# Kernel tuning notes

Measured on AMD Instinct MI355X. Metric: run time of the kernel, lower is better.

The kernel has to match this reference:

```python
import jax, jax.numpy as jnp
import numpy as np

B, S, D, H, F = 8, 1024, 1024, 16, 4096
DH = D // H  # 64
EPS = 1e-5


def layer_norm(x, g, b):
    mu = jnp.mean(x, axis=-1, keepdims=True)
    var = jnp.mean(jnp.square(x - mu), axis=-1, keepdims=True)
    return (x - mu) * jax.lax.rsqrt(var + EPS) * g + b


def mha(q_in, k_in, v_in, wq, wk, wv, wo, causal):
    # wq/wk/wv: [H, D, DH] (stacked per-head nn.Linear weights, pre-transposed)
    Q = jnp.einsum('bsd,hdk->bhsk', q_in, wq)
    K = jnp.einsum('bsd,hdk->bhsk', k_in, wk)
    V = jnp.einsum('bsd,hdk->bhsk', v_in, wv)
    scores = jnp.einsum('bhsk,bhtk->bhst', Q, K) / jnp.sqrt(jnp.asarray(DH, Q.dtype))
    if causal:
        mask = jnp.triu(jnp.ones((S, S), dtype=bool), k=1)  # True = inaccessible
        scores = jnp.where(mask, -jnp.inf, scores)
    A = jax.nn.softmax(scores, axis=-1)
    heads = jnp.einsum('bhst,bhtk->bhsk', A, V)
    heads = heads.transpose(0, 2, 1, 3).reshape(q_in.shape[0], q_in.shape[1], D)
    return heads @ wo.T  # nn.Linear convention


def setup_inputs() -> dict:
    key = jax.random.key(0)
    ks = jax.random.split(key, 16)
    sc = 1.0 / np.sqrt(D)
    scf = 1.0 / np.sqrt(F)
    return {
        'embeds': jax.random.normal(ks[0], (B, S, D), jnp.float32),
        'encoder_output': jax.random.normal(ks[1], (B, S, D), jnp.float32),
        'wq1': jax.random.normal(ks[2], (H, D, DH), jnp.float32) * sc,
        'wk1': jax.random.normal(ks[3], (H, D, DH), jnp.float32) * sc,
        'wv1': jax.random.normal(ks[4], (H, D, DH), jnp.float32) * sc,
        'wo1': jax.random.normal(ks[5], (D, D), jnp.float32) * sc,
        'wq2': jax.random.normal(ks[6], (H, D, DH), jnp.float32) * sc,
        'wk2': jax.random.normal(ks[7], (H, D, DH), jnp.float32) * sc,
        'wv2': jax.random.normal(ks[8], (H, D, DH), jnp.float32) * sc,
        'wo2': jax.random.normal(ks[9], (D, D), jnp.float32) * sc,
        'ln1_g': jnp.ones((D,), jnp.float32), 'ln1_b': jnp.zeros((D,), jnp.float32),
        'ln2_g': jnp.ones((D,), jnp.float32), 'ln2_b': jnp.zeros((D,), jnp.float32),
        'ln3_g': jnp.ones((D,), jnp.float32), 'ln3_b': jnp.zeros((D,), jnp.float32),
        'w1': jax.random.normal(ks[10], (F, D), jnp.float32) * sc,
        'b1': jnp.zeros((F,), jnp.float32),
        'w2': jax.random.normal(ks[11], (D, F), jnp.float32) * scf,
        'b2': jnp.zeros((D,), jnp.float32),
    }


def reference(embeds, encoder_output, wq1, wk1, wv1, wo1, wq2, wk2, wv2, wo2,
              ln1_g, ln1_b, ln2_g, ln2_b, ln3_g, ln3_b, w1, b1, w2, b2):
    # masked (causal) self-attention + residual + LN
    sa = mha(embeds, embeds, embeds, wq1, wk1, wv1, wo1, causal=True)
    x1 = layer_norm(sa + embeds, ln1_g, ln1_b)
    # cross-attention (no mask) + residual + LN
    ca = mha(x1, encoder_output, encoder_output, wq2, wk2, wv2, wo2, causal=False)
    x2 = layer_norm(ca + x1, ln2_g, ln2_b)
    # feedforward (Linear -> GELU(exact) -> Linear) + residual + LN
    ff = jax.nn.gelu(x2 @ w1.T + b1, approximate=False) @ w2.T + b2
    return layer_norm(ff + x2, ln3_g, ln3_b)
```

## Files before the change

kernel.cpp:

```cpp
#include <hip/hip_runtime.h>
#include <cstdint>
#include <cstddef>

typedef unsigned short u16;
typedef __attribute__((ext_vector_type(4))) float f32x4;
typedef __attribute__((ext_vector_type(4))) float f4;
typedef __attribute__((ext_vector_type(8))) short short8x;
typedef __attribute__((ext_vector_type(4))) u16 u16x4;
typedef __attribute__((ext_vector_type(8))) u16 u16x8;

#define DEV static __device__ __forceinline__

DEV void gl_lds16(const void* g, void* l) {
  __builtin_amdgcn_global_load_lds(
      (const __attribute__((address_space(1))) unsigned int*)g,
      (__attribute__((address_space(3))) unsigned int*)l, 16, 0, 0);
}

DEV u16 f2bf(float f) {
  unsigned u = __float_as_uint(f);
  u += 0x7fffu + ((u >> 16) & 1u);
  return (u16)(u >> 16);
}


__global__ __launch_bounds__(256) void cast_bf16(const float* __restrict__ X, u16* __restrict__ Y) {
  size_t i = ((size_t)blockIdx.x * 256 + threadIdx.x) * 4;
  f4 v = *(const f4*)(X + i);
  u16x4 y;
#pragma unroll
  for (int j = 0; j < 4; ++j) y[j] = f2bf(v[j]);
  *(u16x4*)(Y + i) = y;
}

__global__ __launch_bounds__(256) void cast_wqkv(const float* __restrict__ W, u16* __restrict__ Wt) {
  __shared__ float tile[64][65];
  const int t = threadIdx.x;
  const int h = blockIdx.y;
  const int d0 = blockIdx.x * 64;
  const float* Wb = W + (size_t)h * (1024 * 64);
  const int di = t >> 2;
  const int j0 = (t & 3) * 16;
#pragma unroll
  for (int c = 0; c < 4; ++c) {
    f4 v = *(const f4*)(Wb + (size_t)(d0 + di) * 64 + j0 + c * 4);
#pragma unroll
    for (int j = 0; j < 4; ++j) tile[di][j0 + c * 4 + j] = v[j];
  }
  __syncthreads();
  const int k = t >> 2;
  const int dd0 = (t & 3) * 16;
  u16x8 o0, o1;
#pragma unroll
  for (int u = 0; u < 8; ++u) o0[u] = f2bf(tile[dd0 + u][k]);
#pragma unroll
  for (int u = 0; u < 8; ++u) o1[u] = f2bf(tile[dd0 + 8 + u][k]);
  u16* dst = Wt + (size_t)(h * 64 + k) * 1024 + d0 + dd0;
  *(u16x8*)(dst) = o0;
  *(u16x8*)(dst + 8) = o1;
}

__global__ __launch_bounds__(256) void transpose_v(const u16* __restrict__ V, u16* __restrict__ Vt,
                                                   int vstride, int voff) {
  __shared__ u16 tile[32][72];
  const int t = threadIdx.x;
  const int bh = blockIdx.y;
  const int s0 = blockIdx.x * 32;
  const u16* Vb = V + (size_t)(bh >> 4) * (1024 * (size_t)vstride) + voff + (bh & 15) * 64;
  const int si = t >> 3, d0 = (t & 7) * 8;
  u16x8 val = *(const u16x8*)(Vb + (size_t)(s0 + si) * vstride + d0);
#pragma unroll
  for (int u = 0; u < 8; ++u) tile[si][d0 + u] = val[u];
  __syncthreads();
  const int d = t >> 2, sj0 = (t & 3) * 8;
  u16x8 o;
#pragma unroll
  for (int u = 0; u < 8; ++u) o[u] = tile[sj0 + u][d];
  *(u16x8*)(Vt + (size_t)bh * (64 * 1024) + (size_t)d * 1024 + s0 + sj0) = o;
}

template <int EPI>
__global__ __launch_bounds__(256, 3) void gemm_bt(const u16* __restrict__ A, const u16* __restrict__ Bt,
                                                  void* __restrict__ C, const float* __restrict__ bias,
                                                  int M, int N, int K, int ldc) {
  __shared__ u16 As[2][128 * 32];
  __shared__ u16 Bs[2][128 * 32];
  const int t = threadIdx.x;
  const int wave = t >> 6, lane = t & 63;
  const int lr = lane & 15, lkg = lane >> 4;
  const int swz = (lr >> 1) & 3;
  const int wr = (wave >> 1) * 64, wc = (wave & 1) * 64;
  const int m0 = blockIdx.y * 128, n0 = blockIdx.x * 128;

  const int schunk = ((t & 3) ^ ((t >> 3) & 3)) << 4;
  const char* gA = (const char*)(A + (size_t)(m0 + (t >> 2)) * K) + schunk;
  const char* gB = (const char*)(Bt + (size_t)(n0 + (t >> 2)) * K) + schunk;
  const size_t rowskip = (size_t)64 * K * 2;

  const f32x4 fzero = {0.f, 0.f, 0.f, 0.f};
  f32x4 acc[4][4];
#pragma unroll
  for (int m = 0; m < 4; ++m)
#pragma unroll
    for (int n = 0; n < 4; ++n) acc[m][n] = fzero;

  const int nk = K >> 5;

  auto stage = [&](int buf, int kt) {
    const size_t kb = (size_t)kt * 64;
    char* la = ((char*)&As[buf][0]) + wave * 1024;
    char* lb = ((char*)&Bs[buf][0]) + wave * 1024;
    gl_lds16(gA + kb, la);
    gl_lds16(gA + kb + rowskip, la + 4096);
    gl_lds16(gB + kb, lb);
    gl_lds16(gB + kb + rowskip, lb + 4096);
  };

  auto compute = [&](int buf) {
    const char* as = (const char*)&As[buf][0];
    const char* bs = (const char*)&Bs[buf][0];
    short8x aF[4], bF[4];
#pragma unroll
    for (int m = 0; m < 4; ++m)
      aF[m] = *(const short8x*)(as + (size_t)(wr + m * 16 + lr) * 64 + ((lkg ^ swz) << 4));
#pragma unroll
    for (int n = 0; n < 4; ++n)
      bF[n] = *(const short8x*)(bs + (size_t)(wc + n * 16 + lr) * 64 + ((lkg ^ swz) << 4));
#pragma unroll
    for (int m = 0; m < 4; ++m)
#pragma unroll
      for (int n = 0; n < 4; ++n)
        acc[m][n] = __builtin_amdgcn_mfma_f32_16x16x32_bf16(aF[m], bF[n], acc[m][n], 0, 0, 0);
  };

  stage(0, 0);
  __syncthreads();
  int cur = 0;
  for (int kt = 0; kt < nk; ++kt) {
    if (kt + 1 < nk) stage(cur ^ 1, kt + 1);
    compute(cur);
    __syncthreads();
    cur ^= 1;
  }

#pragma unroll
  for (int m = 0; m < 4; ++m) {
#pragma unroll
    for (int rr = 0; rr < 4; ++rr) {
      const int gm = m0 + wr + m * 16 + lkg * 4 + rr;
#pragma unroll
      for (int n = 0; n < 4; ++n) {
        const int gn = n0 + wc + n * 16 + lr;
        float v = acc[m][n][rr];
        if (EPI == 2 || EPI == 3) v += bias[gn];
        if (EPI == 2) v = 0.5f * v * (1.0f + erff(v * 0.70710678118654752f));
        if (EPI == 4) v *= 0.125f;
        if (EPI == 5 && gn < 1024) v *= 0.125f;
        if (EPI == 1 || EPI == 3)
          ((float*)C)[(size_t)gm * ldc + gn] = v;
        else
          ((u16*)C)[(size_t)gm * ldc + gn] = f2bf(v);
      }
    }
  }
}

template <int CAUSAL>
__global__ __launch_bounds__(256, 2) void flash_attn(const u16* __restrict__ Q, const u16* __restrict__ Kk,
                                                     const u16* __restrict__ Vt, u16* __restrict__ O,
                                                     int qst) {
  __shared__ u16 Ks[2][64 * 64];
  __shared__ u16 Vs[2][64 * 64];
  __shared__ u16 Ps[4][32 * 72];
  const int t = threadIdx.x;
  const int wave = t >> 6, lane = t & 63;
  const int lr = lane & 15, lkg = lane >> 4, lk = lkg * 8;
  const int sw = lr & 7;
  const int bh = blockIdx.y;
  const size_t base = (size_t)(bh >> 4) * (1024 * (size_t)qst) + (bh & 15) * 64;
  const u16* Qb = Q + base;
  const u16* Kb = Kk + base;
  const u16* Vtb = Vt + (size_t)bh * (64 * 1024);
  u16* Ob = O + (size_t)(bh >> 4) * (1024 * 1024) + (bh & 15) * 64;
  const int qt = blockIdx.x * 128;
  const int qw = qt + wave * 32;

  const f32x4 fzero = {0.f, 0.f, 0.f, 0.f};
  short8x qf[2][2];
#pragma unroll
  for (int rb = 0; rb < 2; ++rb)
#pragma unroll
    for (int kk = 0; kk < 2; ++kk)
      qf[rb][kk] = *(const short8x*)(Qb + (size_t)(qw + rb * 16 + lr) * qst + kk * 32 + lk);

  float m_[2][4], l_[2][4];
  f32x4 o_[2][4];
#pragma unroll
  for (int rb = 0; rb < 2; ++rb) {
#pragma unroll
    for (int rr = 0; rr < 4; ++rr) { m_[rb][rr] = -1e30f; l_[rb][rr] = 0.f; }
#pragma unroll
    for (int db = 0; db < 4; ++db) o_[rb][db] = fzero;
  }

  const int rsel = lane >> 3;
  const int csw = ((lane & 7) ^ rsel) << 4;

  auto stage = [&](int buf, int kv0) {
#pragma unroll
    for (int s = 0; s < 2; ++s) {
      const int row = s * 32 + wave * 8 + rsel;
      gl_lds16((const char*)Kb + (size_t)(kv0 + row) * (size_t)(qst * 2) + csw,
               (char*)&Ks[buf][0] + s * 4096 + wave * 1024);
      gl_lds16((const char*)Vtb + (size_t)row * 2048 + (size_t)kv0 * 2 + csw,
               (char*)&Vs[buf][0] + s * 4096 + wave * 1024);
    }
  };

  const int kv_end = CAUSAL ? (qt + 128) : 1024;
  const int nt = kv_end >> 6;

  stage(0, 0);
  __syncthreads();
  int cur = 0;
  for (int tt = 0; tt < nt; ++tt) {
    const int kv0 = tt * 64;
    if (tt + 1 < nt) stage(cur ^ 1, kv0 + 64);

    const char* ksb = (const char*)&Ks[cur][0];
    const char* vsb = (const char*)&Vs[cur][0];

    short8x kf[4][2];
#pragma unroll
    for (int nb = 0; nb < 4; ++nb) {
      const int row = nb * 16 + lr;
#pragma unroll
      for (int kk = 0; kk < 2; ++kk)
        kf[nb][kk] = *(const short8x*)(ksb + row * 128 + (((kk * 4 + lkg) ^ sw) << 4));
    }

#pragma unroll
    for (int rb = 0; rb < 2; ++rb) {
      f32x4 s[4];
#pragma unroll
      for (int nb = 0; nb < 4; ++nb) {
        s[nb] = __builtin_amdgcn_mfma_f32_16x16x32_bf16(qf[rb][0], kf[nb][0], fzero, 0, 0, 0);
        s[nb] = __builtin_amdgcn_mfma_f32_16x16x32_bf16(qf[rb][1], kf[nb][1], s[nb], 0, 0, 0);
      }
      if (CAUSAL && (kv0 + 63 > qw + rb * 16)) {
#pragma unroll
        for (int rr = 0; rr < 4; ++rr) {
          const int qg = qw + rb * 16 + lkg * 4 + rr;
#pragma unroll
          for (int nb = 0; nb < 4; ++nb)
            if (kv0 + nb * 16 + lr > qg) s[nb][rr] = -1e30f;
        }
      }
#pragma unroll
      for (int rr = 0; rr < 4; ++rr) {
        float mx = fmaxf(fmaxf(s[0][rr], s[1][rr]), fmaxf(s[2][rr], s[3][rr]));
#pragma unroll
        for (int d = 1; d < 16; d <<= 1) mx = fmaxf(mx, __shfl_xor(mx, d, 16));
        const float mold = m_[rb][rr];
        const float mnew = fmaxf(mold, mx);
        float p[4];
#pragma unroll
        for (int nb = 0; nb < 4; ++nb) p[nb] = __expf(s[nb][rr] - mnew);
        float rsum = (p[0] + p[1]) + (p[2] + p[3]);
#pragma unroll
        for (int d = 1; d < 16; d <<= 1) rsum += __shfl_xor(rsum, d, 16);
        const float alpha = __expf(mold - mnew);
        m_[rb][rr] = mnew;
        l_[rb][rr] = l_[rb][rr] * alpha + rsum;
#pragma unroll
        for (int db = 0; db < 4; ++db) o_[rb][db][rr] *= alpha;
        const int prow = rb * 16 + lkg * 4 + rr;
#pragma unroll
        for (int nb = 0; nb < 4; ++nb)
          Ps[wave][prow * 72 + nb * 16 + lr] = f2bf(p[nb]);
      }
    }
    asm volatile("s_waitcnt lgkmcnt(0)" ::: "memory");

    short8x vF[4][2];
#pragma unroll
    for (int db = 0; db < 4; ++db) {
      const int row = db * 16 + lr;
#pragma unroll
      for (int kk = 0; kk < 2; ++kk)
        vF[db][kk] = *(const short8x*)(vsb + row * 128 + (((kk * 4 + lkg) ^ sw) << 4));
    }
#pragma unroll
    for (int rb = 0; rb < 2; ++rb) {
#pragma unroll
      for (int kk = 0; kk < 2; ++kk) {
        const short8x aP = *(const short8x*)((const char*)&Ps[wave][0] + (rb * 16 + lr) * 144 + kk * 64 + lkg * 16);
#pragma unroll
        for (int db = 0; db < 4; ++db)
          o_[rb][db] = __builtin_amdgcn_mfma_f32_16x16x32_bf16(aP, vF[db][kk], o_[rb][db], 0, 0, 0);
      }
    }
    __syncthreads();
    cur ^= 1;
  }

#pragma unroll
  for (int rb = 0; rb < 2; ++rb)
#pragma unroll
    for (int rr = 0; rr < 4; ++rr) {
      const float inv = 1.0f / l_[rb][rr];
      const int qg = qw + rb * 16 + lkg * 4 + rr;
#pragma unroll
      for (int db = 0; db < 4; ++db)
        Ob[(size_t)qg * 1024 + db * 16 + lr] = f2bf(o_[rb][db][rr] * inv);
    }
}

__global__ __launch_bounds__(256) void ln_res(const float* __restrict__ X, const float* __restrict__ R,
                                              const float* __restrict__ gam, const float* __restrict__ bet,
                                              float* __restrict__ oF, u16* __restrict__ oB) {
  __shared__ float red[8];
  const int row = blockIdx.x, t = threadIdx.x;
  const int wave = t >> 6, lane = t & 63;
  const size_t off = (size_t)row * 1024 + t * 4;
  f4 x = *(const f4*)(X + off);
  f4 r = *(const f4*)(R + off);
  float v[4];
  float s = 0.f, sq = 0.f;
#pragma unroll
  for (int j = 0; j < 4; ++j) {
    v[j] = x[j] + r[j];
    s += v[j];
    sq += v[j] * v[j];
  }
#pragma unroll
  for (int d = 1; d < 64; d <<= 1) {
    s += __shfl_xor(s, d, 64);
    sq += __shfl_xor(sq, d, 64);
  }
  if (lane == 0) { red[wave * 2] = s; red[wave * 2 + 1] = sq; }
  __syncthreads();
  s = red[0] + red[2] + red[4] + red[6];
  sq = red[1] + red[3] + red[5] + red[7];
  const float mu = s * (1.0f / 1024.0f);
  const float var = sq * (1.0f / 1024.0f) - mu * mu;
  const float rs = rsqrtf(var + 1e-5f);
  f4 g4 = *(const f4*)(gam + t * 4);
  f4 b4 = *(const f4*)(bet + t * 4);
  f4 y;
#pragma unroll
  for (int j = 0; j < 4; ++j) y[j] = (v[j] - mu) * rs * g4[j] + b4[j];
  *(f4*)(oF + off) = y;
  if (oB) {
    u16x4 yb;
#pragma unroll
    for (int j = 0; j < 4; ++j) yb[j] = f2bf(y[j]);
    *(u16x4*)(oB + off) = yb;
  }
}

extern "C" void kernel_launch(void* const* d_in, const int* in_sizes, int n_in,
                              void* d_out, int out_size, void* d_ws, size_t ws_size,
                              hipStream_t stream) {
  const float* embeds = (const float*)d_in[0];
  const float* enc = (const float*)d_in[1];
  const float* wq1 = (const float*)d_in[2];
  const float* wk1 = (const float*)d_in[3];
  const float* wv1 = (const float*)d_in[4];
  const float* wo1 = (const float*)d_in[5];
  const float* wq2 = (const float*)d_in[6];
  const float* wk2 = (const float*)d_in[7];
  const float* wv2 = (const float*)d_in[8];
  const float* wo2 = (const float*)d_in[9];
  const float* ln1g = (const float*)d_in[10];
  const float* ln1b = (const float*)d_in[11];
  const float* ln2g = (const float*)d_in[12];
  const float* ln2b = (const float*)d_in[13];
  const float* ln3g = (const float*)d_in[14];
  const float* ln3b = (const float*)d_in[15];
  const float* w1 = (const float*)d_in[16];
  const float* b1 = (const float*)d_in[17];
  const float* w2 = (const float*)d_in[18];
  const float* b2 = (const float*)d_in[19];
  float* out = (float*)d_out;
  char* ws = (char*)d_ws;
  const size_t MB = (size_t)1 << 20;

  u16* QKV = (u16*)(ws + 0 * MB);
  u16* Vtb = (u16*)(ws + 48 * MB);
  u16* Hd = (u16*)(ws + 64 * MB);
  float* Of = (float*)(ws + 80 * MB);
  u16* ebf = (u16*)(ws + 112 * MB);
  u16* encb = (u16*)(ws + 128 * MB);
  float* x1f = (float*)(ws + 144 * MB);
  float* x2f = (float*)(ws + 176 * MB);
  u16* Wq1t = (u16*)(ws + 208 * MB);
  u16* Wk1t = (u16*)(ws + 210 * MB);
  u16* Wv1t = (u16*)(ws + 212 * MB);
  u16* Wo1b = (u16*)(ws + 214 * MB);
  u16* Wq2t = (u16*)(ws + 216 * MB);
  u16* Wk2t = (u16*)(ws + 218 * MB);
  u16* Wv2t = (u16*)(ws + 220 * MB);
  u16* Wo2b = (u16*)(ws + 222 * MB);
  u16* W1b = (u16*)(ws + 224 * MB);
  u16* W2b = (u16*)(ws + 232 * MB);
  u16* x1b = ebf;
  u16* x2b = encb;
  u16* Hff = (u16*)(ws + 0 * MB);

  dim3 blk(256);

  cast_bf16<<<8192, blk, 0, stream>>>(embeds, ebf);
  cast_bf16<<<8192, blk, 0, stream>>>(enc, encb);
  cast_wqkv<<<dim3(16, 16), blk, 0, stream>>>(wq1, Wq1t);
  cast_wqkv<<<dim3(16, 16), blk, 0, stream>>>(wk1, Wk1t);
  cast_wqkv<<<dim3(16, 16), blk, 0, stream>>>(wv1, Wv1t);
  cast_wqkv<<<dim3(16, 16), blk, 0, stream>>>(wq2, Wq2t);
  cast_wqkv<<<dim3(16, 16), blk, 0, stream>>>(wk2, Wk2t);
  cast_wqkv<<<dim3(16, 16), blk, 0, stream>>>(wv2, Wv2t);
  cast_bf16<<<1024, blk, 0, stream>>>(wo1, Wo1b);
  cast_bf16<<<1024, blk, 0, stream>>>(wo2, Wo2b);
  cast_bf16<<<4096, blk, 0, stream>>>(w1, W1b);
  cast_bf16<<<4096, blk, 0, stream>>>(w2, W2b);

  gemm_bt<5><<<dim3(24, 64), blk, 0, stream>>>(ebf, Wq1t, QKV, nullptr, 8192, 3072, 1024, 3072);
  transpose_v<<<dim3(32, 128), blk, 0, stream>>>(QKV, Vtb, 3072, 2048);
  flash_attn<1><<<dim3(8, 128), blk, 0, stream>>>(QKV, QKV + 1024, Vtb, Hd, 3072);
  gemm_bt<1><<<dim3(8, 64), blk, 0, stream>>>(Hd, Wo1b, Of, nullptr, 8192, 1024, 1024, 1024);
  ln_res<<<8192, blk, 0, stream>>>(Of, embeds, ln1g, ln1b, x1f, x1b);

  gemm_bt<4><<<dim3(8, 64), blk, 0, stream>>>(x1b, Wq2t, QKV, nullptr, 8192, 1024, 1024, 3072);
  gemm_bt<0><<<dim3(16, 64), blk, 0, stream>>>(encb, Wk2t, QKV + 1024, nullptr, 8192, 2048, 1024, 3072);
  transpose_v<<<dim3(32, 128), blk, 0, stream>>>(QKV, Vtb, 3072, 2048);
  flash_attn<0><<<dim3(8, 128), blk, 0, stream>>>(QKV, QKV + 1024, Vtb, Hd, 3072);
  gemm_bt<1><<<dim3(8, 64), blk, 0, stream>>>(Hd, Wo2b, Of, nullptr, 8192, 1024, 1024, 1024);
  ln_res<<<8192, blk, 0, stream>>>(Of, x1f, ln2g, ln2b, x2f, x2b);

  gemm_bt<2><<<dim3(32, 64), blk, 0, stream>>>(x2b, W1b, Hff, b1, 8192, 4096, 1024, 4096);
  gemm_bt<3><<<dim3(8, 64), blk, 0, stream>>>(Hff, W2b, Of, b2, 8192, 1024, 4096, 1024);
  ln_res<<<8192, blk, 0, stream>>>(Of, x2f, ln3g, ln3b, out, nullptr);
}
```

Baseline: 762.8 us.

## Remap GEMM workgroups across XCDs and unroll double-buffered K loop by two

The GEMM now remaps the flat workgroup index so that consecutive tiles land on the same XCD chiplet, which should improve L2 reuse of A/B panels. The K loop is manually unrolled by two with fixed LDS buffers and precomputed read/write pointers, removing per-iteration buffer index arithmetic. ln_res gains an optional bias argument, but every call passes nullptr. The remap assumes the workgroup count is divisible by 8, and the unroll assumes K is a multiple of 64.

```diff
diff --git a/kernel.cpp b/kernel.cpp
--- a/kernel.cpp
+++ b/kernel.cpp
@@ -82,20 +82,39 @@
 template <int EPI>
 __global__ __launch_bounds__(256, 3) void gemm_bt(const u16* __restrict__ A, const u16* __restrict__ Bt,
                                                   void* __restrict__ C, const float* __restrict__ bias,
-                                                  int M, int N, int K, int ldc) {
-  __shared__ u16 As[2][128 * 32];
-  __shared__ u16 Bs[2][128 * 32];
+                                                  int K, int ldc) {
+  __shared__ u16 As0[128 * 32], Bs0[128 * 32];
+  __shared__ u16 As1[128 * 32], Bs1[128 * 32];
   const int t = threadIdx.x;
   const int wave = t >> 6, lane = t & 63;
   const int lr = lane & 15, lkg = lane >> 4;
   const int swz = (lr >> 1) & 3;
   const int wr = (wave >> 1) * 64, wc = (wave & 1) * 64;
-  const int m0 = blockIdx.y * 128, n0 = blockIdx.x * 128;
+
+  const int gx = gridDim.x;
+  const int nwg = gx * gridDim.y;
+  const int flat = blockIdx.y * gx + blockIdx.x;
+  const int wg = (flat & 7) * (nwg >> 3) + (flat >> 3);
+  const int m0 = (wg / gx) * 128, n0 = (wg % gx) * 128;
 
   const int schunk = ((t & 3) ^ ((t >> 3) & 3)) << 4;
-  const char* gA = (const char*)(A + (size_t)(m0 + (t >> 2)) * K) + schunk;
-  const char* gB = (const char*)(Bt + (size_t)(n0 + (t >> 2)) * K) + schunk;
   const size_t rowskip = (size_t)64 * K * 2;
+  const char* gA0 = (const char*)(A + (size_t)(m0 + (t >> 2)) * K) + schunk;
+  const char* gA1 = gA0 + rowskip;
+  const char* gB0 = (const char*)(Bt + (size_t)(n0 + (t >> 2)) * K) + schunk;
+  const char* gB1 = gB0 + rowskip;
+
+  char* dA0 = (char*)As0 + wave * 1024;
+  char* dB0 = (char*)Bs0 + wave * 1024;
+  char* dA1 = (char*)As1 + wave * 1024;
+  char* dB1 = (char*)Bs1 + wave * 1024;
+
+  const int aoff = (wr + lr) * 64 + ((lkg ^ swz) << 4);
+  const int boff = (wc + lr) * 64 + ((lkg ^ swz) << 4);
+  const char* rA0 = (const char*)As0 + aoff;
+  const char* rB0 = (const char*)Bs0 + boff;
+  const char* rA1 = (const char*)As1 + aoff;
+  const char* rB1 = (const char*)Bs1 + boff;
 
   const f32x4 fzero = {0.f, 0.f, 0.f, 0.f};
   f32x4 acc[4][4];
@@ -104,28 +123,12 @@
 #pragma unroll
     for (int n = 0; n < 4; ++n) acc[m][n] = fzero;
 
-  const int nk = K >> 5;
-
-  auto stage = [&](int buf, int kt) {
-    const size_t kb = (size_t)kt * 64;
-    char* la = ((char*)&As[buf][0]) + wave * 1024;
-    char* lb = ((char*)&Bs[buf][0]) + wave * 1024;
-    gl_lds16(gA + kb, la);
-    gl_lds16(gA + kb + rowskip, la + 4096);
-    gl_lds16(gB + kb, lb);
-    gl_lds16(gB + kb + rowskip, lb + 4096);
-  };
-
-  auto compute = [&](int buf) {
-    const char* as = (const char*)&As[buf][0];
-    const char* bs = (const char*)&Bs[buf][0];
+  auto compute = [&](const char* rA, const char* rB) {
     short8x aF[4], bF[4];
 #pragma unroll
-    for (int m = 0; m < 4; ++m)
-      aF[m] = *(const short8x*)(as + (size_t)(wr + m * 16 + lr) * 64 + ((lkg ^ swz) << 4));
-#pragma unroll
-    for (int n = 0; n < 4; ++n)
-      bF[n] = *(const short8x*)(bs + (size_t)(wc + n * 16 + lr) * 64 + ((lkg ^ swz) << 4));
+    for (int m = 0; m < 4; ++m) aF[m] = *(const short8x*)(rA + m * 1024);
+#pragma unroll
+    for (int n = 0; n < 4; ++n) bF[n] = *(const short8x*)(rB + n * 1024);
 #pragma unroll
     for (int m = 0; m < 4; ++m)
 #pragma unroll
@@ -133,14 +136,25 @@
         acc[m][n] = __builtin_amdgcn_mfma_f32_16x16x32_bf16(aF[m], bF[n], acc[m][n], 0, 0, 0);
   };
 
-  stage(0, 0);
+  gl_lds16(gA0, dA0); gl_lds16(gA1, dA0 + 4096);
+  gl_lds16(gB0, dB0); gl_lds16(gB1, dB0 + 4096);
+  gA0 += 64; gA1 += 64; gB0 += 64; gB1 += 64;
   __syncthreads();
-  int cur = 0;
-  for (int kt = 0; kt < nk; ++kt) {
-    if (kt + 1 < nk) stage(cur ^ 1, kt + 1);
-    compute(cur);
+
+  const int nk2 = K >> 6;
+  for (int p = 0; p < nk2; ++p) {
+    gl_lds16(gA0, dA1); gl_lds16(gA1, dA1 + 4096);
+    gl_lds16(gB0, dB1); gl_lds16(gB1, dB1 + 4096);
+    gA0 += 64; gA1 += 64; gB0 += 64; gB1 += 64;
+    compute(rA0, rB0);
     __syncthreads();
-    cur ^= 1;
+    if (p + 1 < nk2) {
+      gl_lds16(gA0, dA0); gl_lds16(gA1, dA0 + 4096);
+      gl_lds16(gB0, dB0); gl_lds16(gB1, dB0 + 4096);
+    }
+    gA0 += 64; gA1 += 64; gB0 += 64; gB1 += 64;
+    compute(rA1, rB1);
+    __syncthreads();
   }
 
 #pragma unroll
@@ -316,7 +330,8 @@
     }
 }
 
-__global__ __launch_bounds__(256) void ln_res(const float* __restrict__ X, const float* __restrict__ R,
+__global__ __launch_bounds__(256) void ln_res(const float* __restrict__ X, const float* __restrict__ bias,
+                                              const float* __restrict__ R,
                                               const float* __restrict__ gam, const float* __restrict__ bet,
                                               float* __restrict__ oF, u16* __restrict__ oB) {
   __shared__ float red[8];
@@ -326,13 +341,16 @@
   f4 x = *(const f4*)(X + off);
   f4 r = *(const f4*)(R + off);
   float v[4];
+#pragma unroll
+  for (int j = 0; j < 4; ++j) v[j] = x[j] + r[j];
+  if (bias) {
+    f4 bb = *(const f4*)(bias + t * 4);
+#pragma unroll
+    for (int j = 0; j < 4; ++j) v[j] += bb[j];
+  }
   float s = 0.f, sq = 0.f;
 #pragma unroll
-  for (int j = 0; j < 4; ++j) {
-    v[j] = x[j] + r[j];
-    s += v[j];
-    sq += v[j] * v[j];
-  }
+  for (int j = 0; j < 4; ++j) { s += v[j]; sq += v[j] * v[j]; }
 #pragma unroll
   for (int d = 1; d < 64; d <<= 1) {
     s += __shfl_xor(s, d, 64);
@@ -423,20 +441,20 @@
   cast_bf16<<<4096, blk, 0, stream>>>(w1, W1b);
   cast_bf16<<<4096, blk, 0, stream>>>(w2, W2b);
 
-  gemm_bt<5><<<dim3(24, 64), blk, 0, stream>>>(ebf, Wq1t, QKV, nullptr, 8192, 3072, 1024, 3072);
+  gemm_bt<5><<<dim3(24, 64), blk, 0, stream>>>(ebf, Wq1t, QKV, nullptr, 1024, 3072);
   transpose_v<<<dim3(32, 128), blk, 0, stream>>>(QKV, Vtb, 3072, 2048);
   flash_attn<1><<<dim3(8, 128), blk, 0, stream>>>(QKV, QKV + 1024, Vtb, Hd, 3072);
-  gemm_bt<1><<<dim3(8, 64), blk, 0, stream>>>(Hd, Wo1b, Of, nullptr, 8192, 1024, 1024, 1024);
-  ln_res<<<8192, blk, 0, stream>>>(Of, embeds, ln1g, ln1b, x1f, x1b);
-
-  gemm_bt<4><<<dim3(8, 64), blk, 0, stream>>>(x1b, Wq2t, QKV, nullptr, 8192, 1024, 1024, 3072);
-  gemm_bt<0><<<dim3(16, 64), blk, 0, stream>>>(encb, Wk2t, QKV + 1024, nullptr, 8192, 2048, 1024, 3072);
+  gemm_bt<1><<<dim3(8, 64), blk, 0, stream>>>(Hd, Wo1b, Of, nullptr, 1024, 1024);
+  ln_res<<<8192, blk, 0, stream>>>(Of, nullptr, embeds, ln1g, ln1b, x1f, x1b);
+
+  gemm_bt<4><<<dim3(8, 64), blk, 0, stream>>>(x1b, Wq2t, QKV, nullptr, 1024, 3072);
+  gemm_bt<0><<<dim3(16, 64), blk, 0, stream>>>(encb, Wk2t, QKV + 1024, nullptr, 1024, 3072);
   transpose_v<<<dim3(32, 128), blk, 0, stream>>>(QKV, Vtb, 3072, 2048);
   flash_attn<0><<<dim3(8, 128), blk, 0, stream>>>(QKV, QKV + 1024, Vtb, Hd, 3072);
-  gemm_bt<1><<<dim3(8, 64), blk, 0, stream>>>(Hd, Wo2b, Of, nullptr, 8192, 1024, 1024, 1024);
-  ln_res<<<8192, blk, 0, stream>>>(Of, x1f, ln2g, ln2b, x2f, x2b);
-
-  gemm_bt<2><<<dim3(32, 64), blk, 0, stream>>>(x2b, W1b, Hff, b1, 8192, 4096, 1024, 4096);
-  gemm_bt<3><<<dim3(8, 64), blk, 0, stream>>>(Hff, W2b, Of, b2, 8192, 1024, 4096, 1024);
-  ln_res<<<8192, blk, 0, stream>>>(Of, x2f, ln3g, ln3b, out, nullptr);
-}
+  gemm_bt<1><<<dim3(8, 64), blk, 0, stream>>>(Hd, Wo2b, Of, nullptr, 1024, 1024);
+  ln_res<<<8192, blk, 0, stream>>>(Of, nullptr, x1f, ln2g, ln2b, x2f, x2b);
+
+  gemm_bt<2><<<dim3(32, 64), blk, 0, stream>>>(x2b, W1b, Hff, b1, 1024, 4096);
+  gemm_bt<3><<<dim3(8, 64), blk, 0, stream>>>(Hff, W2b, Of, b2, 4096, 1024);
+  ln_res<<<8192, blk, 0, stream>>>(Of, nullptr, x2f, ln3g, ln3b, out, nullptr);
+}
```

Result: faster. 719.5 us (-5.7%).
